# Kernel optimization log

Hardware: AMD Instinct MI355X
Metric: run time of the kernel (lower is better)

The kernel has to match this reference:

```python
import jax, jax.numpy as jnp
import numpy as np

B, S, D = 4, 2048, 1024
NH, NKV = 16, 4
DK = D // NH          # 64
NG = NH // NKV        # 4


def _rope_tables(seq, d_k):
    theta = 1.0 / jnp.power(10000.0, jnp.arange(0, d_k, 2, dtype=jnp.float32) / d_k)
    ang = jnp.outer(jnp.arange(seq, dtype=jnp.float32), theta)  # [S, DK/2]
    ang = jnp.concatenate([ang, ang], axis=-1)                   # [S, DK]
    return jnp.cos(ang), jnp.sin(ang)


def _rotate_half(t):
    half = t.shape[-1] // 2
    return jnp.concatenate([-t[..., half:], t[..., :half]], axis=-1)


def _apply_rope(t, cos, sin):
    # t: [B, H, S, DK]; cos/sin: [S, DK]
    return t * cos + _rotate_half(t) * sin


def setup_inputs() -> dict:
    key = jax.random.key(0)
    ks = jax.random.split(key, 5)
    sc = 0.02
    x = jax.random.normal(ks[0], (B, S, D), dtype=jnp.float32)
    Wq = jax.random.normal(ks[1], (D, NH * DK), dtype=jnp.float32) * sc
    Wk = jax.random.normal(ks[2], (D, NKV * DK), dtype=jnp.float32) * sc
    Wv = jax.random.normal(ks[3], (D, NKV * DK), dtype=jnp.float32) * sc
    Wo = jax.random.normal(ks[4], (D, D), dtype=jnp.float32) * sc
    mask = jnp.tril(jnp.ones((S, S), dtype=bool))[None, None]  # causal [1,1,S,S]
    return {"x": x, "Wq": Wq, "Wk": Wk, "Wv": Wv, "Wo": Wo, "mask": mask}


def reference(x, Wq, Wk, Wv, Wo, mask):
    batch, seq, _ = x.shape
    q = (x @ Wq).reshape(batch, seq, NH, DK).transpose(0, 2, 1, 3)    # [B,NH,S,DK]
    k = (x @ Wk).reshape(batch, seq, NKV, DK).transpose(0, 2, 1, 3)   # [B,NKV,S,DK]
    v = (x @ Wv).reshape(batch, seq, NKV, DK).transpose(0, 2, 1, 3)

    cos, sin = _rope_tables(seq, DK)
    q = _apply_rope(q, cos, sin)
    k = _apply_rope(k, cos, sin)

    # GQA: repeat_interleave K/V along head dim
    k = jnp.repeat(k, NG, axis=1)  # [B,NH,S,DK]
    v = jnp.repeat(v, NG, axis=1)

    scores = jnp.einsum('bhqd,bhkd->bhqk', q, k) / jnp.sqrt(jnp.float32(DK))
    scores = jnp.where(mask, scores, jnp.float32(-jnp.inf))
    weights = jax.nn.softmax(scores, axis=-1)
    out = jnp.einsum('bhqk,bhkd->bhqd', weights, v)          # [B,NH,S,DK]
    out = out.transpose(0, 2, 1, 3).reshape(batch, seq, D)   # [B,S,D]
    return out @ Wo
```

## Files before the change

### kernel.cpp

```cpp
#include <hip/hip_runtime.h>

#define DEV __device__ __forceinline__

typedef short s16x8 __attribute__((ext_vector_type(8)));
typedef float f32x4 __attribute__((ext_vector_type(4)));


DEV unsigned short f2bf(float f) {
  union { float f; unsigned int u; } a; a.f = f;
  unsigned int u = a.u;
  u = (u + 0x7FFFu + ((u >> 16) & 1u)) >> 16;
  return (unsigned short)u;
}

DEV unsigned int bfpack2(float a, float b) {
  union { float f; unsigned int u; } x, y; x.f = a; y.f = b;
  return ((x.u + 0x8000u) >> 16) | ((y.u + 0x8000u) & 0xFFFF0000u);
}

DEV unsigned int pktrunc(float a, float b) {
  union { float f; unsigned int u; } x, y; x.f = a; y.f = b;
  return __builtin_amdgcn_perm(y.u, x.u, 0x07060302u);
}

DEV void gl_lds16(const void* g, void* l) {
  __builtin_amdgcn_global_load_lds(
      (const __attribute__((address_space(1))) unsigned int*)g,
      (__attribute__((address_space(3))) unsigned int*)l, 16, 0, 0);
}

__global__ __launch_bounds__(256) void prep_kern(const float* __restrict__ x,
                                                 const float* __restrict__ Wq,
                                                 const float* __restrict__ Wk,
                                                 const float* __restrict__ Wv,
                                                 const float* __restrict__ Wo,
                                                 unsigned short* __restrict__ xb,
                                                 unsigned short* __restrict__ WqkvT,
                                                 unsigned short* __restrict__ WoT) {
  int bid = blockIdx.x;
  if (bid < 8192) {
    int i = bid * 256 + threadIdx.x;
    float4 v = ((const float4*)x)[i];
    ushort4 o = make_ushort4(f2bf(v.x), f2bf(v.y), f2bf(v.z), f2bf(v.w));
    ((ushort4*)xb)[i] = o;
    return;
  }
  int tb = bid - 8192;
  int k0 = (tb & 31) * 32, n0 = (tb >> 5) * 32;
  __shared__ float tile[32][33];
  const float* src; int sc, nloc, drow;
  unsigned short* dst;
  if (n0 < 1024)      { src = Wq; sc = 1024; nloc = n0;        dst = WqkvT; drow = n0; }
  else if (n0 < 1280) { src = Wk; sc = 256;  nloc = n0 - 1024; dst = WqkvT; drow = n0; }
  else if (n0 < 1536) { src = Wv; sc = 256;  nloc = n0 - 1280; dst = WqkvT; drow = n0; }
  else                { src = Wo; sc = 1024; nloc = n0 - 1536; dst = WoT;   drow = n0 - 1536; }
  int tx = threadIdx.x & 31, ty = threadIdx.x >> 5;
  #pragma unroll
  for (int i = ty; i < 32; i += 8)
    tile[i][tx] = src[(k0 + i) * sc + (nloc + tx)];
  __syncthreads();
  #pragma unroll
  for (int i = ty; i < 32; i += 8)
    dst[(size_t)(drow + i) * 1024 + (k0 + tx)] = f2bf(tile[tx][i]);
}

template <int EPI>
__global__ __launch_bounds__(256, 4) void gemm128(
    const unsigned short* __restrict__ A,
    const unsigned short* __restrict__ BT,
    unsigned short* __restrict__ Qbuf,
    unsigned short* __restrict__ Kbuf,
    unsigned short* __restrict__ VTbuf,
    float* __restrict__ Cout) {
  __shared__ __align__(16) unsigned short As[2][128 * 32];
  __shared__ __align__(16) unsigned short Bs[2][128 * 32];
  const int K = 1024;
  const int NKT = K / 32;
  int m0 = blockIdx.x * 128, n0 = blockIdx.y * 128;
  int tid = threadIdx.x, w = tid >> 6, lane = tid & 63;
  int c4 = lane & 15, quad = lane >> 4;
  int x3 = c4 & 3;
  int m_off = (w & 1) * 64, n_off = (w >> 1) * 64;

  f32x4 acc[4][4];
  #pragma unroll
  for (int i = 0; i < 4; i++)
    #pragma unroll
    for (int j = 0; j < 4; j++) acc[i][j] = (f32x4){0.f, 0.f, 0.f, 0.f};

  const unsigned short* pA[2];
  const unsigned short* pB[2];
  #pragma unroll
  for (int i = 0; i < 2; ++i) {
    int slot = i * 256 + tid;
    int row = slot >> 2, cs = slot & 3, lc = cs ^ (row & 3);
    pA[i] = A + (size_t)(m0 + row) * K + lc * 8;
    pB[i] = BT + (size_t)(n0 + row) * K + lc * 8;
  }

  #pragma unroll
  for (int i = 0; i < 2; ++i) {
    int slot = i * 256 + tid;
    gl_lds16(pA[i], (char*)As[0] + slot * 16);
    gl_lds16(pB[i], (char*)Bs[0] + slot * 16);
    pA[i] += 32; pB[i] += 32;
  }

  int cc = (quad ^ x3) * 16;
  for (int kt = 0; kt < NKT; ++kt) {
    int cur = kt & 1, nxt = cur ^ 1;
    __syncthreads();

    if (kt + 1 < NKT) {
      #pragma unroll
      for (int i = 0; i < 2; ++i) {
        int slot = i * 256 + tid;
        gl_lds16(pA[i], (char*)As[nxt] + slot * 16);
        gl_lds16(pB[i], (char*)Bs[nxt] + slot * 16);
        pA[i] += 32; pB[i] += 32;
      }
    }

    s16x8 a[4], b[4];
    #pragma unroll
    for (int mi = 0; mi < 4; ++mi)
      a[mi] = *(const s16x8*)((const char*)As[cur] + (m_off + mi * 16 + c4) * 64 + cc);
    #pragma unroll
    for (int ni = 0; ni < 4; ++ni)
      b[ni] = *(const s16x8*)((const char*)Bs[cur] + (n_off + ni * 16 + c4) * 64 + cc);
    #pragma unroll
    for (int mi = 0; mi < 4; ++mi)
      #pragma unroll
      for (int ni = 0; ni < 4; ++ni)
        acc[mi][ni] = __builtin_amdgcn_mfma_f32_16x16x32_bf16(a[mi], b[ni], acc[mi][ni], 0, 0, 0);
  }

  if (EPI == 1) {
    #pragma unroll
    for (int mi = 0; mi < 4; ++mi)
      #pragma unroll
      for (int ni = 0; ni < 4; ++ni)
        #pragma unroll
        for (int r = 0; r < 4; ++r) {
          int row = m0 + m_off + mi * 16 + quad * 4 + r;
          int col = n0 + n_off + ni * 16 + c4;
          Cout[(size_t)row * 1024 + col] = acc[mi][ni][r];
        }
  } else {
    int colbase = n0 + n_off;
    if (colbase < 1280) {
      const float CTH = 0.41524101186092029f;
      const float SC = 0.18033688011112042f;
      float th0 = exp2f(-(float)c4 * CTH);
      float th1 = exp2f(-(float)(c4 + 16) * CTH);
      bool isQ = colbase < 1024;
      float osc = isQ ? SC : 1.0f;
      #pragma unroll
      for (int mi = 0; mi < 4; ++mi)
        #pragma unroll
        for (int r = 0; r < 4; ++r) {
          int row = m0 + m_off + mi * 16 + quad * 4 + r;
          float pos = (float)(row & 2047);
          float a0 = pos * th0, a1 = pos * th1;
          float c0 = __cosf(a0), s0 = __sinf(a0);
          float c1 = __cosf(a1), s1 = __sinf(a1);
          float v0 = acc[mi][0][r], v1 = acc[mi][1][r];
          float v2 = acc[mi][2][r], v3 = acc[mi][3][r];
          float o0 = (v0 * c0 - v2 * s0) * osc;
          float o1 = (v1 * c1 - v3 * s1) * osc;
          float o2 = (v2 * c0 + v0 * s0) * osc;
          float o3 = (v3 * c1 + v1 * s1) * osc;
          if (isQ) {
            size_t base = (size_t)row * 1024 + colbase + c4;
            Qbuf[base] = f2bf(o0); Qbuf[base + 16] = f2bf(o1);
            Qbuf[base + 32] = f2bf(o2); Qbuf[base + 48] = f2bf(o3);
          } else {
            size_t base = (size_t)row * 256 + (colbase - 1024) + c4;
            Kbuf[base] = f2bf(o0); Kbuf[base + 16] = f2bf(o1);
            Kbuf[base + 32] = f2bf(o2); Kbuf[base + 48] = f2bf(o3);
          }
        }
    } else {
      #pragma unroll
      for (int mi = 0; mi < 4; ++mi)
        #pragma unroll
        for (int ni = 0; ni < 4; ++ni) {
          int row = m0 + m_off + mi * 16 + quad * 4;
          int c = colbase + ni * 16 + c4 - 1280;
          int bb = row >> 11, s = row & 2047;
          uint2 pv = make_uint2(bfpack2(acc[mi][ni][0], acc[mi][ni][1]),
                                bfpack2(acc[mi][ni][2], acc[mi][ni][3]));
          *(uint2*)(VTbuf + ((size_t)(bb * 256 + c)) * 2048 + s) = pv;
        }
    }
  }
}

__global__ __launch_bounds__(256, 3) void attn_kern(
    const unsigned short* __restrict__ Qbuf,
    const unsigned short* __restrict__ Kbuf,
    const unsigned short* __restrict__ VTbuf,
    unsigned short* __restrict__ Obuf) {
  __shared__ __align__(16) unsigned short Ks[2][64 * 64];
  __shared__ __align__(16) unsigned short VTs[2][64 * 64];
  __shared__ __align__(16) unsigned short Ps[4 * 32 * 64];

  int pr = blockIdx.x;
  int g = blockIdx.y >> 1;
  int hp = blockIdx.y & 1;
  int b = blockIdx.z;
  int tid = threadIdx.x, w = tid >> 6, lane = tid & 63;
  int h = g * 4 + hp * 2 + (w >> 1);
  int qh = w & 1;
  int c4 = lane & 15, quad = lane >> 4;
  int x7 = c4 & 7;
  unsigned short* Pw = Ps + w * 2048;

  const unsigned short* kB[2];
  const unsigned short* vB[2];
  #pragma unroll
  for (int i = 0; i < 2; ++i) {
    int L = i * 256 + tid;
    int row = L >> 3, cs = (L & 7) ^ (row & 7);
    kB[i] = Kbuf + (size_t)(b * 2048 + row) * 256 + g * 64 + cs * 8;
    vB[i] = VTbuf + (size_t)(b * 256 + g * 64 + row) * 2048 + cs * 8;
  }

  for (int ph = 0; ph < 2; ++ph) {
    int qtile = ph ? (31 - pr) : pr;
    int nkv = qtile + 1;
    int q0 = qtile * 64;

    s16x8 bq[2][2];
    #pragma unroll
    for (int gg = 0; gg < 2; ++gg)
      #pragma unroll
      for (int kk = 0; kk < 2; ++kk)
        bq[gg][kk] = *(const s16x8*)(Qbuf +
            (size_t)(b * 2048 + q0 + qh * 32 + gg * 16 + c4) * 1024 +
            h * 64 + kk * 32 + quad * 8);

    const unsigned short* kS[2];
    const unsigned short* vS[2];
    #pragma unroll
    for (int i = 0; i < 2; ++i) { kS[i] = kB[i]; vS[i] = vB[i]; }

    f32x4 Oacc[2][4];
    float lacc[2] = {0.f, 0.f};
    #pragma unroll
    for (int gg = 0; gg < 2; ++gg)
      #pragma unroll
      for (int nd = 0; nd < 4; ++nd) Oacc[gg][nd] = (f32x4){0.f, 0.f, 0.f, 0.f};

    __syncthreads();
    #pragma unroll
    for (int i = 0; i < 2; ++i) {
      int L = i * 256 + tid;
      gl_lds16(kS[i], (char*)Ks[0] + L * 16);
      gl_lds16(vS[i], (char*)VTs[0] + L * 16);
      kS[i] += 64 * 256; vS[i] += 64;
    }

    for (int kt = 0; kt < nkv; ++kt) {
      int cur = kt & 1, nxt = cur ^ 1;
      __syncthreads();

      if (kt + 1 < nkv) {
        #pragma unroll
        for (int i = 0; i < 2; ++i) {
          int L = i * 256 + tid;
          gl_lds16(kS[i], (char*)Ks[nxt] + L * 16);
          gl_lds16(vS[i], (char*)VTs[nxt] + L * 16);
          kS[i] += 64 * 256; vS[i] += 64;
        }
      }

      const char* Kc = (const char*)Ks[cur];
      const char* Vc = (const char*)VTs[cur];

      f32x4 st[2][4];
      #pragma unroll
      for (int gg = 0; gg < 2; ++gg)
        #pragma unroll
        for (int mt = 0; mt < 4; ++mt) st[gg][mt] = (f32x4){0.f, 0.f, 0.f, 0.f};
      #pragma unroll
      for (int kk = 0; kk < 2; ++kk) {
        #pragma unroll
        for (int mt = 0; mt < 4; ++mt) {
          s16x8 ak = *(const s16x8*)(Kc + (mt * 16 + c4) * 128 +
                                     ((kk * 4 + quad) ^ x7) * 16);
          st[0][mt] = __builtin_amdgcn_mfma_f32_16x16x32_bf16(ak, bq[0][kk], st[0][mt], 0, 0, 0);
          st[1][mt] = __builtin_amdgcn_mfma_f32_16x16x32_bf16(ak, bq[1][kk], st[1][mt], 0, 0, 0);
        }
      }

      #pragma unroll
      for (int gg = 0; gg < 2; ++gg) {
        int qmin = q0 + qh * 32 + gg * 16;
        if (kt * 64 + 63 > qmin) {
          int qi = qmin + c4;
          #pragma unroll
          for (int mt = 0; mt < 4; ++mt)
            #pragma unroll
            for (int r = 0; r < 4; ++r) {
              int kv = kt * 64 + mt * 16 + quad * 4 + r;
              if (kv > qi) st[gg][mt][r] = -1e30f;
            }
        }
        int rr = gg * 16 + c4;
        #pragma unroll
        for (int mt = 0; mt < 4; ++mt) {
          float e0 = exp2f(st[gg][mt][0]);
          float e1 = exp2f(st[gg][mt][1]);
          float e2 = exp2f(st[gg][mt][2]);
          float e3 = exp2f(st[gg][mt][3]);
          lacc[gg] += (e0 + e1) + (e2 + e3);
          unsigned int lo = pktrunc(e0, e1);
          unsigned int hi = pktrunc(e2, e3);
          int cc = (mt * 2 + (quad >> 1)) ^ x7;
          *(uint2*)((char*)Pw + rr * 128 + cc * 16 + (quad & 1) * 8) =
              make_uint2(lo, hi);
        }
      }

      #pragma unroll
      for (int kk = 0; kk < 2; ++kk) {
        s16x8 ap0 = *(const s16x8*)((const char*)Pw + c4 * 128 +
                                    ((kk * 4 + quad) ^ x7) * 16);
        s16x8 ap1 = *(const s16x8*)((const char*)Pw + (16 + c4) * 128 +
                                    ((kk * 4 + quad) ^ x7) * 16);
        #pragma unroll
        for (int nd = 0; nd < 4; ++nd) {
          s16x8 av = *(const s16x8*)(Vc + (nd * 16 + c4) * 128 +
                                     ((kk * 4 + quad) ^ x7) * 16);
          Oacc[0][nd] = __builtin_amdgcn_mfma_f32_16x16x32_bf16(av, ap0, Oacc[0][nd], 0, 0, 0);
          Oacc[1][nd] = __builtin_amdgcn_mfma_f32_16x16x32_bf16(av, ap1, Oacc[1][nd], 0, 0, 0);
        }
      }
    }

    #pragma unroll
    for (int gg = 0; gg < 2; ++gg) {
      float ls = lacc[gg];
      ls += __shfl_xor(ls, 16);
      ls += __shfl_xor(ls, 32);
      float linv = 1.f / ls;
      int rr = gg * 16 + c4;
      #pragma unroll
      for (int nd = 0; nd < 4; ++nd) {
        unsigned int lo = bfpack2(Oacc[gg][nd][0] * linv, Oacc[gg][nd][1] * linv);
        unsigned int hi = bfpack2(Oacc[gg][nd][2] * linv, Oacc[gg][nd][3] * linv);
        int cc = (nd * 2 + (quad >> 1)) ^ x7;
        *(uint2*)((char*)Pw + rr * 128 + cc * 16 + (quad & 1) * 8) =
            make_uint2(lo, hi);
      }
    }
    {
      int row = lane >> 1;
      int grow = b * 2048 + q0 + qh * 32 + row;
      #pragma unroll
      for (int j = 0; j < 4; ++j) {
        int cb = (lane & 1) * 4 + j;
        uint4 v = *(const uint4*)((const char*)Pw + row * 128 +
                                  (cb ^ (row & 7)) * 16);
        *(uint4*)(Obuf + (size_t)grow * 1024 + h * 64 + cb * 8) = v;
      }
    }
  }
}

extern "C" void kernel_launch(void* const* d_in, const int* in_sizes, int n_in,
                              void* d_out, int out_size, void* d_ws, size_t ws_size,
                              hipStream_t stream) {
  const float* x  = (const float*)d_in[0];
  const float* Wq = (const float*)d_in[1];
  const float* Wk = (const float*)d_in[2];
  const float* Wv = (const float*)d_in[3];
  const float* Wo = (const float*)d_in[4];
  float* out = (float*)d_out;

  unsigned short* xb    = (unsigned short*)d_ws;
  unsigned short* WqkvT = xb + 8192 * 1024;
  unsigned short* WoT   = WqkvT + 1536 * 1024;
  unsigned short* Qbuf  = WoT + 1024 * 1024;
  unsigned short* Kbuf  = Qbuf + 8192 * 1024;
  unsigned short* VTbuf = Kbuf + 8192 * 256;
  unsigned short* Obuf  = VTbuf + 4 * 256 * 2048;

  prep_kern<<<8192 + 2560, 256, 0, stream>>>(x, Wq, Wk, Wv, Wo, xb, WqkvT, WoT);

  gemm128<0><<<dim3(64, 12), 256, 0, stream>>>(xb, WqkvT, Qbuf, Kbuf, VTbuf, nullptr);
  attn_kern<<<dim3(16, 8, 4), 256, 0, stream>>>(Qbuf, Kbuf, VTbuf, Obuf);
  gemm128<1><<<dim3(64, 8), 256, 0, stream>>>(Obuf, WoT, nullptr, nullptr, nullptr, out);
}
```

Measured before the change: 232.7 us.

## Split output GEMM into 128x64 tiles and interleave softmax with PV MFMAs

The output projection GEMM now has its own kernel with 128x64 tiles, doubling the grid from 512 to 1024 blocks so more CUs are busy on the 8192x1024 output. In the attention loop, softmax and the PV MFMAs for the two 16-row query groups are now interleaved: group 0's exp/store and PV multiply run before group 1's softmax. This lets exponentials overlap matrix work, and the V fragments are loaded once and kept in registers for reuse. It raises register pressure from the held V fragments, and the smaller output tiles reuse less data per block.

```diff
diff --git a/kernel.cpp b/kernel.cpp
--- a/kernel.cpp
+++ b/kernel.cpp
@@ -64,14 +64,12 @@
     dst[(size_t)(drow + i) * 1024 + (k0 + tx)] = f2bf(tile[tx][i]);
 }
 
-template <int EPI>
-__global__ __launch_bounds__(256, 4) void gemm128(
+__global__ __launch_bounds__(256, 4) void gemm_qkv(
     const unsigned short* __restrict__ A,
     const unsigned short* __restrict__ BT,
     unsigned short* __restrict__ Qbuf,
     unsigned short* __restrict__ Kbuf,
-    unsigned short* __restrict__ VTbuf,
-    float* __restrict__ Cout) {
+    unsigned short* __restrict__ VTbuf) {
   __shared__ __align__(16) unsigned short As[2][128 * 32];
   __shared__ __align__(16) unsigned short Bs[2][128 * 32];
   const int K = 1024;
@@ -110,7 +108,6 @@
   for (int kt = 0; kt < NKT; ++kt) {
     int cur = kt & 1, nxt = cur ^ 1;
     __syncthreads();
-
     if (kt + 1 < NKT) {
       #pragma unroll
       for (int i = 0; i < 2; ++i) {
@@ -120,7 +117,6 @@
         pA[i] += 32; pB[i] += 32;
       }
     }
-
     s16x8 a[4], b[4];
     #pragma unroll
     for (int mi = 0; mi < 4; ++mi)
@@ -135,65 +131,132 @@
         acc[mi][ni] = __builtin_amdgcn_mfma_f32_16x16x32_bf16(a[mi], b[ni], acc[mi][ni], 0, 0, 0);
   }
 
-  if (EPI == 1) {
-    #pragma unroll
-    for (int mi = 0; mi < 4; ++mi)
-      #pragma unroll
-      for (int ni = 0; ni < 4; ++ni)
-        #pragma unroll
-        for (int r = 0; r < 4; ++r) {
-          int row = m0 + m_off + mi * 16 + quad * 4 + r;
-          int col = n0 + n_off + ni * 16 + c4;
-          Cout[(size_t)row * 1024 + col] = acc[mi][ni][r];
-        }
+  int colbase = n0 + n_off;
+  if (colbase < 1280) {
+    const float CTH = 0.41524101186092029f;
+    const float SC = 0.18033688011112042f;
+    float th0 = exp2f(-(float)c4 * CTH);
+    float th1 = exp2f(-(float)(c4 + 16) * CTH);
+    bool isQ = colbase < 1024;
+    float osc = isQ ? SC : 1.0f;
+    #pragma unroll
+    for (int mi = 0; mi < 4; ++mi)
+      #pragma unroll
+      for (int r = 0; r < 4; ++r) {
+        int row = m0 + m_off + mi * 16 + quad * 4 + r;
+        float pos = (float)(row & 2047);
+        float a0 = pos * th0, a1 = pos * th1;
+        float c0 = __cosf(a0), s0 = __sinf(a0);
+        float c1 = __cosf(a1), s1 = __sinf(a1);
+        float v0 = acc[mi][0][r], v1 = acc[mi][1][r];
+        float v2 = acc[mi][2][r], v3 = acc[mi][3][r];
+        float o0 = (v0 * c0 - v2 * s0) * osc;
+        float o1 = (v1 * c1 - v3 * s1) * osc;
+        float o2 = (v2 * c0 + v0 * s0) * osc;
+        float o3 = (v3 * c1 + v1 * s1) * osc;
+        if (isQ) {
+          size_t base = (size_t)row * 1024 + colbase + c4;
+          Qbuf[base] = f2bf(o0); Qbuf[base + 16] = f2bf(o1);
+          Qbuf[base + 32] = f2bf(o2); Qbuf[base + 48] = f2bf(o3);
+        } else {
+          size_t base = (size_t)row * 256 + (colbase - 1024) + c4;
+          Kbuf[base] = f2bf(o0); Kbuf[base + 16] = f2bf(o1);
+          Kbuf[base + 32] = f2bf(o2); Kbuf[base + 48] = f2bf(o3);
+        }
+      }
   } else {
-    int colbase = n0 + n_off;
-    if (colbase < 1280) {
-      const float CTH = 0.41524101186092029f;
-      const float SC = 0.18033688011112042f;
-      float th0 = exp2f(-(float)c4 * CTH);
-      float th1 = exp2f(-(float)(c4 + 16) * CTH);
-      bool isQ = colbase < 1024;
-      float osc = isQ ? SC : 1.0f;
-      #pragma unroll
-      for (int mi = 0; mi < 4; ++mi)
-        #pragma unroll
-        for (int r = 0; r < 4; ++r) {
-          int row = m0 + m_off + mi * 16 + quad * 4 + r;
-          float pos = (float)(row & 2047);
-          float a0 = pos * th0, a1 = pos * th1;
-          float c0 = __cosf(a0), s0 = __sinf(a0);
-          float c1 = __cosf(a1), s1 = __sinf(a1);
-          float v0 = acc[mi][0][r], v1 = acc[mi][1][r];
-          float v2 = acc[mi][2][r], v3 = acc[mi][3][r];
-          float o0 = (v0 * c0 - v2 * s0) * osc;
-          float o1 = (v1 * c1 - v3 * s1) * osc;
-          float o2 = (v2 * c0 + v0 * s0) * osc;
-          float o3 = (v3 * c1 + v1 * s1) * osc;
-          if (isQ) {
-            size_t base = (size_t)row * 1024 + colbase + c4;
-            Qbuf[base] = f2bf(o0); Qbuf[base + 16] = f2bf(o1);
-            Qbuf[base + 32] = f2bf(o2); Qbuf[base + 48] = f2bf(o3);
-          } else {
-            size_t base = (size_t)row * 256 + (colbase - 1024) + c4;
-            Kbuf[base] = f2bf(o0); Kbuf[base + 16] = f2bf(o1);
-            Kbuf[base + 32] = f2bf(o2); Kbuf[base + 48] = f2bf(o3);
-          }
-        }
-    } else {
-      #pragma unroll
-      for (int mi = 0; mi < 4; ++mi)
-        #pragma unroll
-        for (int ni = 0; ni < 4; ++ni) {
-          int row = m0 + m_off + mi * 16 + quad * 4;
-          int c = colbase + ni * 16 + c4 - 1280;
-          int bb = row >> 11, s = row & 2047;
-          uint2 pv = make_uint2(bfpack2(acc[mi][ni][0], acc[mi][ni][1]),
-                                bfpack2(acc[mi][ni][2], acc[mi][ni][3]));
-          *(uint2*)(VTbuf + ((size_t)(bb * 256 + c)) * 2048 + s) = pv;
-        }
-    }
-  }
+    #pragma unroll
+    for (int mi = 0; mi < 4; ++mi)
+      #pragma unroll
+      for (int ni = 0; ni < 4; ++ni) {
+        int row = m0 + m_off + mi * 16 + quad * 4;
+        int c = colbase + ni * 16 + c4 - 1280;
+        int bb = row >> 11, s = row & 2047;
+        uint2 pv = make_uint2(bfpack2(acc[mi][ni][0], acc[mi][ni][1]),
+                              bfpack2(acc[mi][ni][2], acc[mi][ni][3]));
+        *(uint2*)(VTbuf + ((size_t)(bb * 256 + c)) * 2048 + s) = pv;
+      }
+  }
+}
+
+__global__ __launch_bounds__(256, 4) void gemm_out(
+    const unsigned short* __restrict__ A,
+    const unsigned short* __restrict__ BT,
+    float* __restrict__ Cout) {
+  __shared__ __align__(16) unsigned short As[2][128 * 32];
+  __shared__ __align__(16) unsigned short Bs[2][64 * 32];
+  const int K = 1024;
+  const int NKT = K / 32;
+  int m0 = blockIdx.x * 128, n0 = blockIdx.y * 64;
+  int tid = threadIdx.x, w = tid >> 6, lane = tid & 63;
+  int c4 = lane & 15, quad = lane >> 4;
+  int x3 = c4 & 3;
+  int m_off = (w & 1) * 64, n_off = (w >> 1) * 32;
+
+  f32x4 acc[4][2];
+  #pragma unroll
+  for (int i = 0; i < 4; i++)
+    #pragma unroll
+    for (int j = 0; j < 2; j++) acc[i][j] = (f32x4){0.f, 0.f, 0.f, 0.f};
+
+  const unsigned short* pA[2];
+  const unsigned short* pB;
+  #pragma unroll
+  for (int i = 0; i < 2; ++i) {
+    int slot = i * 256 + tid;
+    int row = slot >> 2, cs = slot & 3, lc = cs ^ (row & 3);
+    pA[i] = A + (size_t)(m0 + row) * K + lc * 8;
+  }
+  {
+    int row = tid >> 2, cs = (tid & 3) ^ ((tid >> 2) & 3);
+    pB = BT + (size_t)(n0 + row) * K + cs * 8;
+  }
+
+  #pragma unroll
+  for (int i = 0; i < 2; ++i) {
+    gl_lds16(pA[i], (char*)As[0] + (i * 256 + tid) * 16);
+    pA[i] += 32;
+  }
+  gl_lds16(pB, (char*)Bs[0] + tid * 16);
+  pB += 32;
+
+  int cc = (quad ^ x3) * 16;
+  for (int kt = 0; kt < NKT; ++kt) {
+    int cur = kt & 1, nxt = cur ^ 1;
+    __syncthreads();
+    if (kt + 1 < NKT) {
+      #pragma unroll
+      for (int i = 0; i < 2; ++i) {
+        gl_lds16(pA[i], (char*)As[nxt] + (i * 256 + tid) * 16);
+        pA[i] += 32;
+      }
+      gl_lds16(pB, (char*)Bs[nxt] + tid * 16);
+      pB += 32;
+    }
+    s16x8 a[4], b[2];
+    #pragma unroll
+    for (int mi = 0; mi < 4; ++mi)
+      a[mi] = *(const s16x8*)((const char*)As[cur] + (m_off + mi * 16 + c4) * 64 + cc);
+    #pragma unroll
+    for (int ni = 0; ni < 2; ++ni)
+      b[ni] = *(const s16x8*)((const char*)Bs[cur] + (n_off + ni * 16 + c4) * 64 + cc);
+    #pragma unroll
+    for (int mi = 0; mi < 4; ++mi)
+      #pragma unroll
+      for (int ni = 0; ni < 2; ++ni)
+        acc[mi][ni] = __builtin_amdgcn_mfma_f32_16x16x32_bf16(a[mi], b[ni], acc[mi][ni], 0, 0, 0);
+  }
+
+  #pragma unroll
+  for (int mi = 0; mi < 4; ++mi)
+    #pragma unroll
+    for (int ni = 0; ni < 2; ++ni)
+      #pragma unroll
+      for (int r = 0; r < 4; ++r) {
+        int row = m0 + m_off + mi * 16 + quad * 4 + r;
+        int col = n0 + n_off + ni * 16 + c4;
+        Cout[(size_t)row * 1024 + col] = acc[mi][ni][r];
+      }
 }
 
 __global__ __launch_bounds__(256, 3) void attn_kern(
@@ -294,48 +357,77 @@
         }
       }
 
-      #pragma unroll
-      for (int gg = 0; gg < 2; ++gg) {
-        int qmin = q0 + qh * 32 + gg * 16;
-        if (kt * 64 + 63 > qmin) {
-          int qi = qmin + c4;
+      bool diag = (kt * 64 + 63 > q0 + qh * 32);
+      s16x8 avr[2][4];
+
+      {
+        if (diag) {
+          int qi = q0 + qh * 32 + c4;
           #pragma unroll
           for (int mt = 0; mt < 4; ++mt)
             #pragma unroll
             for (int r = 0; r < 4; ++r) {
               int kv = kt * 64 + mt * 16 + quad * 4 + r;
-              if (kv > qi) st[gg][mt][r] = -1e30f;
+              if (kv > qi) st[0][mt][r] = -1e30f;
             }
         }
-        int rr = gg * 16 + c4;
         #pragma unroll
         for (int mt = 0; mt < 4; ++mt) {
-          float e0 = exp2f(st[gg][mt][0]);
-          float e1 = exp2f(st[gg][mt][1]);
-          float e2 = exp2f(st[gg][mt][2]);
-          float e3 = exp2f(st[gg][mt][3]);
-          lacc[gg] += (e0 + e1) + (e2 + e3);
+          float e0 = exp2f(st[0][mt][0]);
+          float e1 = exp2f(st[0][mt][1]);
+          float e2 = exp2f(st[0][mt][2]);
+          float e3 = exp2f(st[0][mt][3]);
+          lacc[0] += (e0 + e1) + (e2 + e3);
           unsigned int lo = pktrunc(e0, e1);
           unsigned int hi = pktrunc(e2, e3);
           int cc = (mt * 2 + (quad >> 1)) ^ x7;
-          *(uint2*)((char*)Pw + rr * 128 + cc * 16 + (quad & 1) * 8) =
+          *(uint2*)((char*)Pw + c4 * 128 + cc * 16 + (quad & 1) * 8) =
               make_uint2(lo, hi);
         }
       }
-
       #pragma unroll
       for (int kk = 0; kk < 2; ++kk) {
         s16x8 ap0 = *(const s16x8*)((const char*)Pw + c4 * 128 +
                                     ((kk * 4 + quad) ^ x7) * 16);
+        #pragma unroll
+        for (int nd = 0; nd < 4; ++nd) {
+          avr[kk][nd] = *(const s16x8*)(Vc + (nd * 16 + c4) * 128 +
+                                        ((kk * 4 + quad) ^ x7) * 16);
+          Oacc[0][nd] = __builtin_amdgcn_mfma_f32_16x16x32_bf16(avr[kk][nd], ap0, Oacc[0][nd], 0, 0, 0);
+        }
+      }
+      {
+        if (diag) {
+          int qi = q0 + qh * 32 + 16 + c4;
+          #pragma unroll
+          for (int mt = 0; mt < 4; ++mt)
+            #pragma unroll
+            for (int r = 0; r < 4; ++r) {
+              int kv = kt * 64 + mt * 16 + quad * 4 + r;
+              if (kv > qi) st[1][mt][r] = -1e30f;
+            }
+        }
+        #pragma unroll
+        for (int mt = 0; mt < 4; ++mt) {
+          float e0 = exp2f(st[1][mt][0]);
+          float e1 = exp2f(st[1][mt][1]);
+          float e2 = exp2f(st[1][mt][2]);
+          float e3 = exp2f(st[1][mt][3]);
+          lacc[1] += (e0 + e1) + (e2 + e3);
+          unsigned int lo = pktrunc(e0, e1);
+          unsigned int hi = pktrunc(e2, e3);
+          int cc = (mt * 2 + (quad >> 1)) ^ x7;
+          *(uint2*)((char*)Pw + (16 + c4) * 128 + cc * 16 + (quad & 1) * 8) =
+              make_uint2(lo, hi);
+        }
+      }
+      #pragma unroll
+      for (int kk = 0; kk < 2; ++kk) {
         s16x8 ap1 = *(const s16x8*)((const char*)Pw + (16 + c4) * 128 +
                                     ((kk * 4 + quad) ^ x7) * 16);
         #pragma unroll
-        for (int nd = 0; nd < 4; ++nd) {
-          s16x8 av = *(const s16x8*)(Vc + (nd * 16 + c4) * 128 +
-                                     ((kk * 4 + quad) ^ x7) * 16);
-          Oacc[0][nd] = __builtin_amdgcn_mfma_f32_16x16x32_bf16(av, ap0, Oacc[0][nd], 0, 0, 0);
-          Oacc[1][nd] = __builtin_amdgcn_mfma_f32_16x16x32_bf16(av, ap1, Oacc[1][nd], 0, 0, 0);
-        }
+        for (int nd = 0; nd < 4; ++nd)
+          Oacc[1][nd] = __builtin_amdgcn_mfma_f32_16x16x32_bf16(avr[kk][nd], ap1, Oacc[1][nd], 0, 0, 0);
       }
     }
 
@@ -389,7 +481,7 @@
 
   prep_kern<<<8192 + 2560, 256, 0, stream>>>(x, Wq, Wk, Wv, Wo, xb, WqkvT, WoT);
 
-  gemm128<0><<<dim3(64, 12), 256, 0, stream>>>(xb, WqkvT, Qbuf, Kbuf, VTbuf, nullptr);
+  gemm_qkv<<<dim3(64, 12), 256, 0, stream>>>(xb, WqkvT, Qbuf, Kbuf, VTbuf);
   attn_kern<<<dim3(16, 8, 4), 256, 0, stream>>>(Qbuf, Kbuf, VTbuf, Obuf);
-  gemm128<1><<<dim3(64, 8), 256, 0, stream>>>(Obuf, WoT, nullptr, nullptr, nullptr, out);
-}
+  gemm_out<<<dim3(64, 16), 256, 0, stream>>>(Obuf, WoT, out);
+}
```

After: 241.4 us. 3.7% more time.
